# Kernel optimization log

Hardware: AMD Instinct MI355X
Metric: run time of the kernel (lower is better)

Reference implementation:

```python
import jax, jax.numpy as jnp
import numpy as np

BN_EPS = 1e-5


def _poly_ste(x):
    # Piecewise polynomial surrogate used for the activation STE backward:
    #   x < -1        -> -1
    #   x >= 1        -> 1
    out = jnp.where(x < -1, -1.0, x * x + 2.0 * x)
    out = jnp.where(x < 0, out, -x * x + 2.0 * x)
    out = jnp.where(x < 1, out, 1.0)
    return out


def setup_inputs() -> dict:
    key = jax.random.key(0)
    ks = jax.random.split(key, 7)
    N, C, H, W = 32, 128, 56, 56
    P = 128  # planes
    return {
        "x": jax.random.normal(ks[0], (N, C, H, W), dtype=jnp.float32),
        "weight": jax.random.normal(ks[1], (P, C, 3, 3), dtype=jnp.float32) * 0.05,
        "bias": jax.random.normal(ks[2], (P,), dtype=jnp.float32) * 0.05,
        "gamma": jax.random.uniform(ks[3], (P,), dtype=jnp.float32, minval=0.5, maxval=1.5),
        "beta": jax.random.normal(ks[4], (P,), dtype=jnp.float32) * 0.05,
        "running_mean": jax.random.normal(ks[5], (P,), dtype=jnp.float32) * 0.1,
        "running_var": jax.random.uniform(ks[6], (P,), dtype=jnp.float32, minval=0.5, maxval=1.5),
    }


def reference(x, weight, bias, gamma, beta, running_mean, running_var):
    # BinaryActivation: forward = sign(x), backward = d(poly)/dx (STE via detach trick)
    poly = _poly_ste(x)
    a = poly + jax.lax.stop_gradient(jnp.sign(x) - poly)

    # HardBinaryConv: weights binarized with straight-through sign; input already +/-1.
    wb = weight + jax.lax.stop_gradient(jnp.sign(weight) - weight)

    # 3x3 conv, stride 1, padding 1, NCHW / OIHW layout
    out = jax.lax.conv_general_dilated(
        a, wb,
        window_strides=(1, 1),
        padding=((1, 1), (1, 1)),
        dimension_numbers=("NCHW", "OIHW", "NCHW"),
    )
    out = out + bias[None, :, None, None]

    # BatchNorm2d in eval mode (running statistics)
    inv = gamma / jnp.sqrt(running_var + BN_EPS)
    out = out * inv[None, :, None, None] + (beta - running_mean * inv)[None, :, None, None]

    # Residual add (downsample=None, stride=1, inplanes==planes)
    return out + x
```

## Files before the change

kernel.cpp:

```cpp
#include <hip/hip_runtime.h>
#include <stdint.h>

#define N_  32
#define C_  128
#define H_  56
#define W_  56
#define HW_ 3136
#define P_  128

using i32x4 = __attribute__((ext_vector_type(4))) int;

#define WI8_BYTES (P_*1152)

__global__ __launch_bounds__(256) void wpack_kernel(const float* __restrict__ weight,
        const float* __restrict__ bias, const float* __restrict__ gamma,
        const float* __restrict__ beta, const float* __restrict__ mean,
        const float* __restrict__ var,
        uint32_t* __restrict__ wI8, float* __restrict__ invG, float* __restrict__ b0G) {
    int gid = blockIdx.x * 256 + threadIdx.x;
    int p   = gid / 288;
    int rem = gid % 288;
    int k   = rem * 4;
    int tp  = k >> 7;
    int c   = k & 127;
    uint32_t d = 0;
    #pragma unroll
    for (int i2 = 0; i2 < 4; ++i2) {
        float v = weight[((size_t)p * C_ + c + i2) * 9 + tp];
        uint32_t by = (v >= 0.f) ? 0x01u : 0xFFu;
        d |= by << (8 * i2);
    }
    wI8[gid] = d;
    if (blockIdx.x == 0 && threadIdx.x < P_) {
        int pp = threadIdx.x;
        float inv = gamma[pp] * rsqrtf(var[pp] + 1e-5f);
        invG[pp] = inv;
        b0G[pp]  = bias[pp] * inv + beta[pp] - mean[pp] * inv;
    }
}

__global__ __launch_bounds__(256) void bconv_kernel(
        const uint4* __restrict__ wI8v,
        const float* __restrict__ invG, const float* __restrict__ b0G,
        const float* __restrict__ x, float* __restrict__ out) {
    __shared__ uint4 actT[4 * 68 * 8];
    __shared__ float sInv[P_], sB0[P_];

    int tid = threadIdx.x;
    int bid = (blockIdx.x & 7) * 112 + (blockIdx.x >> 3);
    int img = bid / 28;
    int rp  = bid % 28;
    int r0  = rp * 2;

    int lane = tid & 63;
    int wi   = tid >> 6;
    int q    = lane >> 4;
    int l15  = lane & 15;
    int m0   = wi * 32;

    if (tid < P_) { sInv[tid] = invG[tid]; sB0[tid] = b0G[tid]; }

    if (tid < 224) {
        int rho = tid / 56;
        int rr  = tid % 56;
        int cg  = rr / 14;
        int tq  = rr % 14;
        int h   = r0 - 1 + rho;
        bool vh = ((unsigned)h < (unsigned)H_);
        uint32_t c0 = vh ? 0x01010101u : 0u;
        uint32_t cf = vh ? 0xFEu       : 0u;
        const uint32_t* xb = (const uint32_t*)x
            + ((size_t)img * C_ + cg * 32) * HW_ + (vh ? h : 0) * W_ + tq * 4;
        int colL0 = tq * 4 + 1;
        #pragma unroll
        for (int ph = 0; ph < 2; ++ph) {
            uint32_t cell0[4], cell1[4], cell2[4], cell3[4];
            #pragma unroll
            for (int d = 0; d < 4; ++d) {
                uint32_t w0 = 0, w1 = 0, w2 = 0, w3 = 0;
                if (vh) {
                    #pragma unroll
                    for (int i = 0; i < 4; ++i) {
                        uint4 u = *(const uint4*)(xb + (size_t)(ph * 16 + d * 4 + i) * HW_);
                        uint32_t sh = i * 8;
                        w0 |= (u.x >> 31) << sh;
                        w1 |= (u.y >> 31) << sh;
                        w2 |= (u.z >> 31) << sh;
                        w3 |= (u.w >> 31) << sh;
                    }
                }
                cell0[d] = c0 + w0 * cf;
                cell1[d] = c0 + w1 * cf;
                cell2[d] = c0 + w2 * cf;
                cell3[d] = c0 + w3 * cf;
            }
            int cb = cg * 2 + ph;
            actT[(rho * 68 + colL0 + 0) * 8 + (cb ^ ((colL0 + 0) & 7))] =
                make_uint4(cell0[0], cell0[1], cell0[2], cell0[3]);
            actT[(rho * 68 + colL0 + 1) * 8 + (cb ^ ((colL0 + 1) & 7))] =
                make_uint4(cell1[0], cell1[1], cell1[2], cell1[3]);
            actT[(rho * 68 + colL0 + 2) * 8 + (cb ^ ((colL0 + 2) & 7))] =
                make_uint4(cell2[0], cell2[1], cell2[2], cell2[3]);
            actT[(rho * 68 + colL0 + 3) * 8 + (cb ^ ((colL0 + 3) & 7))] =
                make_uint4(cell3[0], cell3[1], cell3[2], cell3[3]);
        }
    } else {
        int z = tid - 224;
        #pragma unroll
        for (int rep = 0; rep < 2; ++rep) {
            int e = z + rep * 32;
            if (e < 48) {
                int rho  = e / 12;
                int jj   = e % 12;
                int colL = jj ? (56 + jj) : 0;
                int base = (rho * 68 + colL) * 8;
                #pragma unroll
                for (int s = 0; s < 8; ++s) actT[base + s] = make_uint4(0u,0u,0u,0u);
            }
        }
    }

    __syncthreads();

    i32x4 acc[2][8];
    #pragma unroll
    for (int mi = 0; mi < 2; ++mi)
        #pragma unroll
        for (int j = 0; j < 8; ++j)
            #pragma unroll
            for (int e = 0; e < 4; ++e) acc[mi][j][e] = 0;

    #pragma unroll 1
    for (int t9 = 0; t9 < 9; ++t9) {
        i32x4 aw[2][2];
        #pragma unroll
        for (int mi = 0; mi < 2; ++mi)
            #pragma unroll
            for (int ks = 0; ks < 2; ++ks)
                aw[mi][ks] = *(const i32x4*)&wI8v[(size_t)(m0 + mi*16 + l15) * 72
                                                  + t9 * 8 + ks * 4 + q];
        int dh = t9 / 3, dw = t9 % 3;
        #pragma unroll
        for (int ks = 0; ks < 2; ++ks) {
            #pragma unroll
            for (int j = 0; j < 8; ++j) {
                int n    = j * 16 + l15;
                int colL = (n & 63) + dw;
                int rho  = (n >> 6) + dh;
                i32x4 bf = *(const i32x4*)&actT[(rho * 68 + colL) * 8 + ((ks * 4 + q) ^ (colL & 7))];
                acc[0][j] = __builtin_amdgcn_mfma_i32_16x16x64_i8(aw[0][ks], bf, acc[0][j], 0, 0, 0);
                acc[1][j] = __builtin_amdgcn_mfma_i32_16x16x64_i8(aw[1][ks], bf, acc[1][j], 0, 0, 0);
            }
        }
    }

    #pragma unroll
    for (int j = 0; j < 8; ++j) {
        int n = j * 16 + l15;
        int w = n & 63;
        if (w < W_) {
            int orow = r0 + (n >> 6);
            size_t pixOff = (size_t)img * P_ * HW_ + (size_t)orow * W_ + w;
            #pragma unroll
            for (int mi = 0; mi < 2; ++mi)
                #pragma unroll
                for (int reg = 0; reg < 4; ++reg) {
                    int m = m0 + mi * 16 + q * 4 + reg;
                    size_t off = pixOff + (size_t)m * HW_;
                    out[off] = (float)acc[mi][j][reg] * sInv[m] + sB0[m] + x[off];
                }
        }
    }
}

extern "C" void kernel_launch(void* const* d_in, const int* in_sizes, int n_in,
                              void* d_out, int out_size, void* d_ws, size_t ws_size,
                              hipStream_t stream) {
    const float* x      = (const float*)d_in[0];
    const float* weight = (const float*)d_in[1];
    const float* bias   = (const float*)d_in[2];
    const float* gamma  = (const float*)d_in[3];
    const float* beta   = (const float*)d_in[4];
    const float* mean   = (const float*)d_in[5];
    const float* var    = (const float*)d_in[6];
    float* out = (float*)d_out;

    uint8_t*  ws    = (uint8_t*)d_ws;
    uint32_t* wI8   = (uint32_t*)ws;
    float*    invG  = (float*)(ws + WI8_BYTES);
    float*    b0G   = invG + P_;

    wpack_kernel<<<144, 256, 0, stream>>>(weight, bias, gamma, beta, mean, var, wI8, invG, b0G);
    bconv_kernel<<<32 * 28, 256, 0, stream>>>((const uint4*)wI8, invG, b0G, x, out);
}
```

Before: 143.7 us.

## Switch binary conv to 32x32x32 int8 MFMA with double-buffered weight fragments

Replaces the 16x16x64 int8 MFMA tiling (2 M-tiles by 8 N-tiles per wave) with 32x32x32 int8 MFMA (one 32-row M-tile by 4 N-tiles of 32 pixels). The larger MFMA shape cuts the number of LDS B-fragment reads per tap and halves the MFMA instruction count. Weight fragments for the next tap are prefetched into a second register buffer while the current tap computes, and the first tap's load is issued before the activation-staging phase. The epilogue also hoists the per-channel BN scale and shift into registers. The cost is a different accumulator-to-channel mapping and higher register pressure from the 16-wide accumulators and the doubled weight buffer.

```diff
diff --git a/kernel.cpp b/kernel.cpp
--- a/kernel.cpp
+++ b/kernel.cpp
@@ -8,7 +8,8 @@
 #define HW_ 3136
 #define P_  128
 
-using i32x4 = __attribute__((ext_vector_type(4))) int;
+using i32x4  = __attribute__((ext_vector_type(4)))  int;
+using i32x16 = __attribute__((ext_vector_type(16))) int;
 
 #define WI8_BYTES (P_*1152)
 
@@ -54,11 +55,17 @@
 
     int lane = tid & 63;
     int wi   = tid >> 6;
-    int q    = lane >> 4;
-    int l15  = lane & 15;
+    int l31  = lane & 31;
+    int kl   = lane >> 5;
     int m0   = wi * 32;
 
     if (tid < P_) { sInv[tid] = invG[tid]; sB0[tid] = b0G[tid]; }
+
+    const uint4* wbase = wI8v + (size_t)(m0 + l31) * 72 + kl;
+    i32x4 aw[2][4];
+    #pragma unroll
+    for (int ks2 = 0; ks2 < 4; ++ks2)
+        aw[0][ks2] = *(const i32x4*)&wbase[ks2 * 2];
 
     if (tid < 224) {
         int rho = tid / 56;
@@ -122,53 +129,55 @@
 
     __syncthreads();
 
-    i32x4 acc[2][8];
-    #pragma unroll
-    for (int mi = 0; mi < 2; ++mi)
-        #pragma unroll
-        for (int j = 0; j < 8; ++j)
-            #pragma unroll
-            for (int e = 0; e < 4; ++e) acc[mi][j][e] = 0;
+    i32x16 acc[4];
+    #pragma unroll
+    for (int t = 0; t < 4; ++t)
+        #pragma unroll
+        for (int e = 0; e < 16; ++e) acc[t][e] = 0;
 
     #pragma unroll 1
     for (int t9 = 0; t9 < 9; ++t9) {
-        i32x4 aw[2][2];
-        #pragma unroll
-        for (int mi = 0; mi < 2; ++mi)
-            #pragma unroll
-            for (int ks = 0; ks < 2; ++ks)
-                aw[mi][ks] = *(const i32x4*)&wI8v[(size_t)(m0 + mi*16 + l15) * 72
-                                                  + t9 * 8 + ks * 4 + q];
+        int nb = t9 & 1;
+        if (t9 < 8) {
+            #pragma unroll
+            for (int ks2 = 0; ks2 < 4; ++ks2)
+                aw[nb ^ 1][ks2] = *(const i32x4*)&wbase[(t9 + 1) * 8 + ks2 * 2];
+        }
         int dh = t9 / 3, dw = t9 % 3;
         #pragma unroll
-        for (int ks = 0; ks < 2; ++ks) {
-            #pragma unroll
-            for (int j = 0; j < 8; ++j) {
-                int n    = j * 16 + l15;
-                int colL = (n & 63) + dw;
-                int rho  = (n >> 6) + dh;
-                i32x4 bf = *(const i32x4*)&actT[(rho * 68 + colL) * 8 + ((ks * 4 + q) ^ (colL & 7))];
-                acc[0][j] = __builtin_amdgcn_mfma_i32_16x16x64_i8(aw[0][ks], bf, acc[0][j], 0, 0, 0);
-                acc[1][j] = __builtin_amdgcn_mfma_i32_16x16x64_i8(aw[1][ks], bf, acc[1][j], 0, 0, 0);
-            }
-        }
-    }
-
-    #pragma unroll
-    for (int j = 0; j < 8; ++j) {
-        int n = j * 16 + l15;
-        int w = n & 63;
+        for (int ks2 = 0; ks2 < 4; ++ks2) {
+            #pragma unroll
+            for (int t = 0; t < 4; ++t) {
+                int pxg  = t * 32 + l31;
+                int colL = (pxg & 63) + dw;
+                int rho  = (pxg >> 6) + dh;
+                i32x4 bf = *(const i32x4*)&actT[(rho * 68 + colL) * 8
+                                                + ((ks2 * 2 + kl) ^ (colL & 7))];
+                acc[t] = __builtin_amdgcn_mfma_i32_32x32x32_i8(aw[nb][ks2], bf, acc[t], 0, 0, 0);
+            }
+        }
+    }
+
+    float invR[16], b0R[16];
+    #pragma unroll
+    for (int reg = 0; reg < 16; ++reg) {
+        int m = m0 + (reg & 3) + 8 * (reg >> 2) + 4 * kl;
+        invR[reg] = sInv[m];
+        b0R[reg]  = sB0[m];
+    }
+    #pragma unroll
+    for (int t = 0; t < 4; ++t) {
+        int pxg = t * 32 + l31;
+        int w   = pxg & 63;
         if (w < W_) {
-            int orow = r0 + (n >> 6);
+            int orow = r0 + (pxg >> 6);
             size_t pixOff = (size_t)img * P_ * HW_ + (size_t)orow * W_ + w;
             #pragma unroll
-            for (int mi = 0; mi < 2; ++mi)
-                #pragma unroll
-                for (int reg = 0; reg < 4; ++reg) {
-                    int m = m0 + mi * 16 + q * 4 + reg;
-                    size_t off = pixOff + (size_t)m * HW_;
-                    out[off] = (float)acc[mi][j][reg] * sInv[m] + sB0[m] + x[off];
-                }
+            for (int reg = 0; reg < 16; ++reg) {
+                int m = m0 + (reg & 3) + 8 * (reg >> 2) + 4 * kl;
+                size_t off = pixOff + (size_t)m * HW_;
+                out[off] = (float)acc[t][reg] * invR[reg] + b0R[reg] + x[off];
+            }
         }
     }
 }
```

After: 176.1 us. 22.5% more time.

## Stage epilogue through LDS for float4 stores and double-buffer weight loads

Applied to the files above, without the earlier changes.

Weight fragments for the next 3x3 tap are now prefetched into a second register buffer while the current tap's MFMAs run, with the first tap loaded before activation staging. The epilogue no longer writes scalar strided floats straight from the MFMA layout. Each wave instead writes its scaled accumulators to a per-wave LDS tile that reuses the activation buffer, then reads them back as float4 rows so the residual load and the output store are coalesced and vectorized. This adds register pressure from the doubled weight buffer and an extra barrier. It also relies on s_waitcnt alone, not a barrier, for intra-wave LDS ordering between the write and the transposed read.

```diff
diff --git a/kernel.cpp b/kernel.cpp
--- a/kernel.cpp
+++ b/kernel.cpp
@@ -60,11 +60,20 @@
 
     if (tid < P_) { sInv[tid] = invG[tid]; sB0[tid] = b0G[tid]; }
 
+    const uint4* wbase = wI8v + (size_t)(m0 + l15) * 72;
+    i32x4 aw[2][2][2];
+    #pragma unroll
+    for (int mi = 0; mi < 2; ++mi)
+        #pragma unroll
+        for (int ks = 0; ks < 2; ++ks)
+            aw[0][mi][ks] = *(const i32x4*)&wI8v[(size_t)(m0 + mi*16 + l15) * 72
+                                                 + ks * 4 + q];
+
     if (tid < 224) {
         int rho = tid / 56;
-        int rr  = tid % 56;
-        int cg  = rr / 14;
-        int tq  = rr % 14;
+        int rr2 = tid % 56;
+        int cg  = rr2 / 14;
+        int tq  = rr2 % 14;
         int h   = r0 - 1 + rho;
         bool vh = ((unsigned)h < (unsigned)H_);
         uint32_t c0 = vh ? 0x01010101u : 0u;
@@ -132,13 +141,15 @@
 
     #pragma unroll 1
     for (int t9 = 0; t9 < 9; ++t9) {
-        i32x4 aw[2][2];
-        #pragma unroll
-        for (int mi = 0; mi < 2; ++mi)
-            #pragma unroll
-            for (int ks = 0; ks < 2; ++ks)
-                aw[mi][ks] = *(const i32x4*)&wI8v[(size_t)(m0 + mi*16 + l15) * 72
-                                                  + t9 * 8 + ks * 4 + q];
+        int nb = t9 & 1;
+        if (t9 < 8) {
+            #pragma unroll
+            for (int mi = 0; mi < 2; ++mi)
+                #pragma unroll
+                for (int ks = 0; ks < 2; ++ks)
+                    aw[nb ^ 1][mi][ks] = *(const i32x4*)&wI8v[(size_t)(m0 + mi*16 + l15) * 72
+                                                              + (t9 + 1) * 8 + ks * 4 + q];
+        }
         int dh = t9 / 3, dw = t9 % 3;
         #pragma unroll
         for (int ks = 0; ks < 2; ++ks) {
@@ -148,28 +159,52 @@
                 int colL = (n & 63) + dw;
                 int rho  = (n >> 6) + dh;
                 i32x4 bf = *(const i32x4*)&actT[(rho * 68 + colL) * 8 + ((ks * 4 + q) ^ (colL & 7))];
-                acc[0][j] = __builtin_amdgcn_mfma_i32_16x16x64_i8(aw[0][ks], bf, acc[0][j], 0, 0, 0);
-                acc[1][j] = __builtin_amdgcn_mfma_i32_16x16x64_i8(aw[1][ks], bf, acc[1][j], 0, 0, 0);
-            }
-        }
-    }
-
-    #pragma unroll
-    for (int j = 0; j < 8; ++j) {
-        int n = j * 16 + l15;
-        int w = n & 63;
-        if (w < W_) {
-            int orow = r0 + (n >> 6);
-            size_t pixOff = (size_t)img * P_ * HW_ + (size_t)orow * W_ + w;
-            #pragma unroll
-            for (int mi = 0; mi < 2; ++mi)
+                acc[0][j] = __builtin_amdgcn_mfma_i32_16x16x64_i8(aw[nb][0][ks], bf, acc[0][j], 0, 0, 0);
+                acc[1][j] = __builtin_amdgcn_mfma_i32_16x16x64_i8(aw[nb][1][ks], bf, acc[1][j], 0, 0, 0);
+            }
+        }
+    }
+
+    __syncthreads();
+
+    float* S = (float*)actT + wi * (16 * 132);
+    #pragma unroll
+    for (int mi = 0; mi < 2; ++mi) {
+        float invR[4], b0R[4];
+        #pragma unroll
+        for (int reg = 0; reg < 4; ++reg) {
+            int m = m0 + mi * 16 + q * 4 + reg;
+            invR[reg] = sInv[m];
+            b0R[reg]  = sB0[m];
+        }
+        #pragma unroll
+        for (int j = 0; j < 8; ++j) {
+            int n = j * 16 + l15;
+            #pragma unroll
+            for (int reg = 0; reg < 4; ++reg)
+                S[(q * 4 + reg) * 132 + n] = (float)acc[mi][j][reg] * invR[reg] + b0R[reg];
+        }
+        asm volatile("s_waitcnt lgkmcnt(0)" ::: "memory");
+        if (lane < 56) {
+            int ch4 = lane / 14;
+            int wq  = lane % 14;
+            #pragma unroll
+            for (int k = 0; k < 4; ++k) {
+                int chl = k * 4 + ch4;
+                int ch  = m0 + mi * 16 + chl;
                 #pragma unroll
-                for (int reg = 0; reg < 4; ++reg) {
-                    int m = m0 + mi * 16 + q * 4 + reg;
-                    size_t off = pixOff + (size_t)m * HW_;
-                    out[off] = (float)acc[mi][j][reg] * sInv[m] + sB0[m] + x[off];
+                for (int rr2 = 0; rr2 < 2; ++rr2) {
+                    float4 v = *(float4*)&S[chl * 132 + rr2 * 64 + wq * 4];
+                    size_t off = (size_t)img * P_ * HW_ + (size_t)ch * HW_
+                               + (size_t)(r0 + rr2) * W_ + wq * 4;
+                    const float4 xr = *(const float4*)&x[off];
+                    v.x += xr.x; v.y += xr.y; v.z += xr.z; v.w += xr.w;
+                    *(float4*)&out[off] = v;
                 }
-        }
+            }
+        }
+        if (mi == 0)
+            asm volatile("s_waitcnt lgkmcnt(0)" ::: "memory");
     }
 }
 
```

Measured after the change: 149.8 us. 1.04x slower.
